# Optimization experiments

Measured on AMD Instinct MI355X. Metric: run time of the kernel, lower is better.

The kernel has to match this reference:

```python
import jax, jax.numpy as jnp
import numpy as np

B, N, D, K, L, NC = 8, 4096, 64, 8, 2, 2
EPS = 1e-5


def setup_inputs() -> dict:
    key = jax.random.key(0)
    ks = iter(jax.random.split(key, 64))
    def p(*shape, s=0.05):
        return jax.random.normal(next(ks), shape, dtype=jnp.float32) * s
    return dict(
        x=p(B, N, 3, s=1.0),
        ew1=p(3, D), eb1=jnp.zeros((D,), jnp.float32), ew2=p(D, D), eb2=jnp.zeros((D,), jnp.float32),
        wq=p(L, D, D), bq=jnp.zeros((L, D), jnp.float32), wk=p(L, D, D), bk=jnp.zeros((L, D), jnp.float32),
        wv=p(L, D, D), bv=jnp.zeros((L, D), jnp.float32),
        pw1=p(L, 3, D), pb1=jnp.zeros((L, D), jnp.float32), pw2=p(L, D, D), pb2=jnp.zeros((L, D), jnp.float32),
        aw=p(L, D), ab=jnp.zeros((L,), jnp.float32),
        ow=p(L, D, D), ob=jnp.zeros((L, D), jnp.float32),
        l1g=jnp.ones((L, D), jnp.float32), l1b=jnp.zeros((L, D), jnp.float32),
        l2g=jnp.ones((L, D), jnp.float32), l2b=jnp.zeros((L, D), jnp.float32),
        fw1=p(L, D, 2 * D), fb1=jnp.zeros((L, 2 * D), jnp.float32),
        fw2=p(L, 2 * D, D), fb2=jnp.zeros((L, D), jnp.float32),
        cw=p(D, 2 * D), cb=jnp.zeros((2 * D,), jnp.float32),
        cg=jnp.ones((2 * D,), jnp.float32), cbeta=jnp.zeros((2 * D,), jnp.float32),
        f1w=p(2 * D, 128), f1b=jnp.zeros((128,), jnp.float32),
        b1g=jnp.ones((128,), jnp.float32), b1b=jnp.zeros((128,), jnp.float32),
        f2w=p(128, 64), f2b=jnp.zeros((64,), jnp.float32),
        b2g=jnp.ones((64,), jnp.float32), b2b=jnp.zeros((64,), jnp.float32),
        f3w=p(64, NC), f3b=jnp.zeros((NC,), jnp.float32),
    )


def _ln(x, g, b):
    m = jnp.mean(x, -1, keepdims=True)
    v = jnp.mean((x - m) ** 2, -1, keepdims=True)
    return g * (x - m) * jax.lax.rsqrt(v + EPS) + b


def _bn(x, g, b):
    # eval-mode BatchNorm with running_mean=0, running_var=1
    return g * x * jax.lax.rsqrt(jnp.float32(1.0 + EPS)) + b


def _knn(pos, k):
    sq = jnp.sum(pos * pos, -1)  # [B,N]
    d2 = sq[:, :, None] - 2.0 * jnp.einsum('bnd,bmd->bnm', pos, pos) + sq[:, None, :]
    _, idx = jax.lax.top_k(-d2, k)  # k smallest distances (includes self)
    return jax.lax.stop_gradient(idx)  # [B,N,k]


def _gather(t, idx):
    b, n, k = idx.shape
    flat = idx.reshape(b, n * k)
    return jnp.take_along_axis(t, flat[:, :, None], axis=1).reshape(b, n, k, t.shape[-1])


def _block(x, pos, idx, pr):
    (wq, bq, wk, bk, wv, bv, pw1, pb1, pw2, pb2, aw, ab,
     ow, ob, l1g, l1b, l2g, l2b, fw1, fb1, fw2, fb2) = pr
    q = x @ wq + bq
    k = x @ wk + bk
    v = x @ wv + bv
    kg = _gather(k, idx)      # [B,N,K,C]
    vg = _gather(v, idx)
    pg = _gather(pos, idx)    # [B,N,K,3]
    pd = pos[:, :, None, :] - pg
    pe = jax.nn.relu(pd @ pw1 + pb1) @ pw2 + pb2
    ai = q[:, :, None, :] - kg + pe  # subtraction attention
    logits = jnp.einsum('bnkc,c->bnk', ai, aw) + ab
    w = jax.nn.softmax(logits, axis=-1)
    out = jnp.einsum('bnk,bnkc->bnc', w, vg + pe)
    out = out @ ow + ob
    out = _ln(out + x, l1g, l1b)
    ffn = jax.nn.gelu(out @ fw1 + fb1, approximate=False) @ fw2 + fb2
    return _ln(out + ffn, l2g, l2b)


def reference(x, ew1, eb1, ew2, eb2, wq, bq, wk, bk, wv, bv, pw1, pb1, pw2, pb2,
              aw, ab, ow, ob, l1g, l1b, l2g, l2b, fw1, fb1, fw2, fb2,
              cw, cb, cg, cbeta, f1w, f1b, b1g, b1b, f2w, f2b, b2g, b2b, f3w, f3b):
    pos = x
    h = jax.nn.relu(x @ ew1 + eb1) @ ew2 + eb2  # [B,N,D]
    idx = _knn(pos, K)
    stacked = (wq, bq, wk, bk, wv, bv, pw1, pb1, pw2, pb2, aw, ab,
               ow, ob, l1g, l1b, l2g, l2b, fw1, fb1, fw2, fb2)
    for i in range(L):
        h = _block(h, pos, idx, tuple(a[i] for a in stacked))
    y = jax.nn.relu(_bn(h @ cw + cb, cg, cbeta))  # [B,N,2D]
    g = jnp.max(y, axis=1)  # global max pool over points
    g = jax.nn.relu(_bn(g @ f1w + f1b, b1g, b1b))
    g = jax.nn.relu(_bn(g @ f2w + f2b, b2g, b2b))
    return g @ f3w + f3b  # [B, NC]
```

## Files before the change

kernel.cpp:

```cpp
#include <hip/hip_runtime.h>
#include <cmath>

#define BB 8
#define NN 4096
#define DD 64
#define KK 8
#define NCLS 2

constexpr float LNEPS = 1e-5f;
constexpr float BNRS = 0.9999950000374994f;
constexpr float INVSQRT2 = 0.70710678118654752440f;

constexpr int QKV_GRID = 512;
constexpr int ATTN_GRID = 1024;
constexpr int FFN_GRID = 512;

#define QPB 64
#define SPLITS 16
#define SUBSET 64

__device__ __forceinline__ float wave_sum(float v) {
#pragma unroll
  for (int m = 32; m > 0; m >>= 1) v += __shfl_xor(v, m, 64);
  return v;
}

__device__ __forceinline__ float gelu_exact(float x) {
  return 0.5f * x * (1.0f + erff(x * INVSQRT2));
}

__device__ __forceinline__ float dist2(float4 q, float4 p) {
  float dot = fmaf(q.x, p.x, fmaf(q.y, p.y, q.z * p.z));
  return fmaf(-2.0f, dot, q.w + p.w);
}

__global__ void zero_kernel(float* g) { g[threadIdx.x] = 0.0f; }

__global__ __launch_bounds__(256) void embed_kernel(
    const float* __restrict__ x, const float* __restrict__ ew1, const float* __restrict__ eb1,
    const float* __restrict__ ew2, const float* __restrict__ eb2, float* __restrict__ h) {
  __shared__ float h1[4][DD];
  int w = threadIdx.x >> 6, c = threadIdx.x & 63;
  int pt = ((blockIdx.x & 7) << 12) + (blockIdx.x >> 3) * 4 + w;
  const float* xp = x + (size_t)pt * 3;
  float x0 = xp[0], x1 = xp[1], x2 = xp[2];
  float a = fmaf(x0, ew1[c], fmaf(x1, ew1[64 + c], fmaf(x2, ew1[128 + c], eb1[c])));
  h1[w][c] = fmaxf(a, 0.0f);
  float s = eb2[c];
#pragma unroll 8
  for (int d = 0; d < DD; d++) s = fmaf(h1[w][d], ew2[d * 64 + c], s);
  h[(size_t)pt * 64 + c] = s;
}

__global__ __launch_bounds__(256) void knn_prep_kernel(const float* __restrict__ x,
                                                       float4* __restrict__ ppg) {
  int i = ((blockIdx.x & 7) << 12) + (blockIdx.x >> 3) * 256 + threadIdx.x;
  float a0 = x[3 * i + 0], a1 = x[3 * i + 1], a2 = x[3 * i + 2];
  ppg[i] = make_float4(a0, a1, a2, a0 * a0 + a1 * a1 + a2 * a2);
}

__global__ __launch_bounds__(1024) void knn_kernel(const float4* __restrict__ ppg,
                                                   int* __restrict__ idx) {
  __shared__ union {
    float v[SPLITS * 8][QPB];
    double k[SPLITS * 8][QPB];
  } mb;
  __shared__ float thrq[QPB];
  int b = blockIdx.x & 7;
  int qbase = (blockIdx.x >> 3) * QPB;
  const float4* pb = ppg + (size_t)b * NN;
  int ql = threadIdx.x & 63;
  int sp = __builtin_amdgcn_readfirstlane(threadIdx.x >> 6);
  float4 qp = pb[qbase + ql];
  const float4* cp = pb + sp * (NN / SPLITS);

  float bd[8];
#pragma unroll
  for (int u = 0; u < 8; u++) bd[u] = INFINITY;
#pragma unroll 4
  for (int jj = 0; jj < SUBSET; ++jj) {
    float d2 = dist2(qp, cp[jj]);
#pragma unroll
    for (int u = 7; u > 0; --u) bd[u] = fminf(bd[u], fmaxf(bd[u - 1], d2));
    bd[0] = fminf(bd[0], d2);
  }
#pragma unroll
  for (int u = 0; u < 8; u++) mb.v[sp * 8 + u][ql] = bd[u];
  __syncthreads();

  if (sp < 8) {
    float cd[8];
#pragma unroll
    for (int u = 0; u < 8; u++) cd[u] = INFINITY;
    int base = sp * 16;
#pragma unroll
    for (int e = 0; e < 16; e++) {
      float vv = mb.v[base + e][ql];
#pragma unroll
      for (int u = 7; u > 0; --u) cd[u] = fminf(cd[u], fmaxf(cd[u - 1], vv));
      cd[0] = fminf(cd[0], vv);
    }
#pragma unroll
    for (int u = 0; u < 8; u++) mb.v[base + u][ql] = cd[u];
  }
  __syncthreads();

  if (sp == 0) {
    float cd[8];
#pragma unroll
    for (int u = 0; u < 8; u++) cd[u] = INFINITY;
    for (int m = 0; m < 8; m++) {
      for (int e = 0; e < 8; e++) {
        float vv = mb.v[m * 16 + e][ql];
        if (__all(vv >= cd[7])) break;
#pragma unroll
        for (int u = 7; u > 0; --u) cd[u] = fminf(cd[u], fmaxf(cd[u - 1], vv));
        cd[0] = fminf(cd[0], vv);
      }
    }
    thrq[ql] = cd[7];
  }
  __syncthreads();
  float U = thrq[ql];

  double kd[8];
#pragma unroll
  for (int u = 0; u < 8; u++) kd[u] = INFINITY;
#pragma unroll 4
  for (int jj = 0; jj < NN / SPLITS; ++jj) {
    float d2 = dist2(qp, cp[jj]);
    if (d2 <= U) {
      double key = __hiloint2double(__float_as_int(d2), sp * (NN / SPLITS) + jj);
      if (key < kd[7]) {
#pragma unroll
        for (int u = 7; u > 0; --u) kd[u] = fmin(kd[u], fmax(kd[u - 1], key));
        kd[0] = fmin(kd[0], key);
      }
    }
  }
#pragma unroll
  for (int u = 0; u < 8; u++) mb.k[sp * 8 + u][ql] = kd[u];
  __syncthreads();

  if (sp < 8) {
    double cd[8];
#pragma unroll
    for (int u = 0; u < 8; u++) cd[u] = INFINITY;
    int base = sp * 16;
#pragma unroll
    for (int e = 0; e < 16; e++) {
      double key = mb.k[base + e][ql];
#pragma unroll
      for (int u = 7; u > 0; --u) cd[u] = fmin(cd[u], fmax(cd[u - 1], key));
      cd[0] = fmin(cd[0], key);
    }
#pragma unroll
    for (int u = 0; u < 8; u++) mb.k[base + u][ql] = cd[u];
  }
  __syncthreads();

  if (sp == 0) {
    double cd[8];
#pragma unroll
    for (int u = 0; u < 8; u++) cd[u] = INFINITY;
    for (int m = 0; m < 8; m++) {
      for (int e = 0; e < 8; e++) {
        double key = mb.k[m * 16 + e][ql];
        if (__all(key >= cd[7])) break;
#pragma unroll
        for (int u = 7; u > 0; --u) cd[u] = fmin(cd[u], fmax(cd[u - 1], key));
        cd[0] = fmin(cd[0], key);
      }
    }
    int* op = idx + ((size_t)b * NN + qbase + ql) * 8;
#pragma unroll
    for (int u = 0; u < 8; u++) op[u] = __double2loint(cd[u]);
  }
}

__global__ __launch_bounds__(256) void qkv_kernel(
    const float* __restrict__ h, const float* __restrict__ wq, const float* __restrict__ bq,
    const float* __restrict__ wk, const float* __restrict__ bk,
    const float* __restrict__ wv, const float* __restrict__ bv,
    float* __restrict__ q, float* __restrict__ k, float* __restrict__ v) {
  __shared__ float lwq[DD * DD], lwk[DD * DD], lwv[DD * DD];
  __shared__ float lbq[DD], lbk[DD], lbv[DD];
  __shared__ __attribute__((aligned(16))) float hb[4][DD][4];
  int tid = threadIdx.x;
  for (int i = tid; i < DD * DD; i += 256) { lwq[i] = wq[i]; lwk[i] = wk[i]; lwv[i] = wv[i]; }
  if (tid < DD) { lbq[tid] = bq[tid]; lbk[tid] = bk[tid]; lbv[tid] = bv[tid]; }
  __syncthreads();
  int w = tid >> 6, c = tid & 63;
  int batch = blockIdx.x & 7, pos = blockIdx.x >> 3;
  constexpr int ITERS = NN / ((QKV_GRID / 8) * 16);
  for (int it = 0; it < ITERS; ++it) {
    int p0 = (batch << 12) + ((it * 64 + pos) * 4 + w) * 4;
#pragma unroll
    for (int i = 0; i < 4; i++) hb[w][c][i] = h[(size_t)(p0 + i) * 64 + c];
    float aq[4], ak[4], av[4];
#pragma unroll
    for (int i = 0; i < 4; i++) { aq[i] = lbq[c]; ak[i] = lbk[c]; av[i] = lbv[c]; }
#pragma unroll 4
    for (int d = 0; d < DD; d++) {
      float wq_ = lwq[d * 64 + c], wk_ = lwk[d * 64 + c], wv_ = lwv[d * 64 + c];
      float4 hh = *(const float4*)&hb[w][d][0];
      aq[0] = fmaf(hh.x, wq_, aq[0]); aq[1] = fmaf(hh.y, wq_, aq[1]);
      aq[2] = fmaf(hh.z, wq_, aq[2]); aq[3] = fmaf(hh.w, wq_, aq[3]);
      ak[0] = fmaf(hh.x, wk_, ak[0]); ak[1] = fmaf(hh.y, wk_, ak[1]);
      ak[2] = fmaf(hh.z, wk_, ak[2]); ak[3] = fmaf(hh.w, wk_, ak[3]);
      av[0] = fmaf(hh.x, wv_, av[0]); av[1] = fmaf(hh.y, wv_, av[1]);
      av[2] = fmaf(hh.z, wv_, av[2]); av[3] = fmaf(hh.w, wv_, av[3]);
    }
#pragma unroll
    for (int i = 0; i < 4; i++) {
      q[(size_t)(p0 + i) * 64 + c] = aq[i];
      k[(size_t)(p0 + i) * 64 + c] = ak[i];
      v[(size_t)(p0 + i) * 64 + c] = av[i];
    }
  }
}

__global__ __launch_bounds__(256) void attn_kernel(
    const float* __restrict__ x, const float* __restrict__ h,
    const float* q, const float* __restrict__ kk, const float* __restrict__ vv,
    const int* __restrict__ idx,
    const float* __restrict__ pw1, const float* __restrict__ pb1,
    const float* __restrict__ pw2, const float* __restrict__ pb2,
    const float* __restrict__ aw, const float* __restrict__ ab,
    const float* __restrict__ ow, const float* __restrict__ ob,
    const float* __restrict__ l1g, const float* __restrict__ l1b,
    float* t) {
  __shared__ float lpw2[DD * DD];
  __shared__ float lpw1[3 * DD], lpb1[DD], lpb2[DD], law[DD], lob_[DD], ll1g[DD], ll1b[DD];
  __shared__ __attribute__((aligned(16))) float h1b[4][2][DD][8];
  __shared__ __attribute__((aligned(16))) float outb[4][2][DD];
  int tid = threadIdx.x;
  for (int i = tid; i < DD * DD; i += 256) lpw2[i] = pw2[i];
  if (tid < 3 * DD) lpw1[tid] = pw1[tid];
  if (tid < DD) {
    lpb1[tid] = pb1[tid]; lpb2[tid] = pb2[tid]; law[tid] = aw[tid];
    lob_[tid] = ob[tid]; ll1g[tid] = l1g[tid]; ll1b[tid] = l1b[tid];
  }
  float lab = ab[0];
  __syncthreads();
  int w = tid >> 6, c = tid & 63;
  int b = blockIdx.x & 7, pos = blockIdx.x >> 3;
  const float* xb = x + (size_t)b * NN * 3;
  constexpr int ITERS = NN / ((ATTN_GRID / 8) * 8);
  for (int it = 0; it < ITERS; ++it) {
    int n0 = ((it * 128 + pos) * 8) + w * 2;
    int p0 = (b << 12) + n0;
    float hs0 = h[(size_t)p0 * 64 + c], hs1 = h[(size_t)(p0 + 1) * 64 + c];
    float qs0 = q[(size_t)p0 * 64 + c], qs1 = q[(size_t)(p0 + 1) * 64 + c];
    int nb[2][8];
#pragma unroll
    for (int u = 0; u < 8; u++) {
      nb[0][u] = idx[(size_t)p0 * 8 + u];
      nb[1][u] = idx[(size_t)(p0 + 1) * 8 + u];
    }
    float kv0[8], kv1[8], vg0[8], vg1[8];
#pragma unroll
    for (int u = 0; u < 8; u++) {
      kv0[u] = kk[((size_t)(b << 12) + nb[0][u]) * 64 + c];
      kv1[u] = kk[((size_t)(b << 12) + nb[1][u]) * 64 + c];
      vg0[u] = vv[((size_t)(b << 12) + nb[0][u]) * 64 + c];
      vg1[u] = vv[((size_t)(b << 12) + nb[1][u]) * 64 + c];
    }
    float w1c0 = lpw1[c], w1c1 = lpw1[64 + c], w1c2 = lpw1[128 + c], b1c = lpb1[c];
#pragma unroll
    for (int pt = 0; pt < 2; ++pt) {
      int n = n0 + pt;
      float px0 = xb[n * 3 + 0], px1 = xb[n * 3 + 1], px2 = xb[n * 3 + 2];
      float h1v[8];
#pragma unroll
      for (int u = 0; u < 8; u++) {
        int m = nb[pt][u];
        float d0 = px0 - xb[m * 3 + 0], d1 = px1 - xb[m * 3 + 1], d2 = px2 - xb[m * 3 + 2];
        h1v[u] = fmaxf(fmaf(d0, w1c0, fmaf(d1, w1c1, fmaf(d2, w1c2, b1c))), 0.0f);
      }
      *(float4*)&h1b[w][pt][c][0] = make_float4(h1v[0], h1v[1], h1v[2], h1v[3]);
      *(float4*)&h1b[w][pt][c][4] = make_float4(h1v[4], h1v[5], h1v[6], h1v[7]);
    }
    float acc0[8], acc1[8];
    float pb2c = lpb2[c];
#pragma unroll
    for (int u = 0; u < 8; u++) { acc0[u] = pb2c; acc1[u] = pb2c; }
#pragma unroll 2
    for (int d = 0; d < DD; d++) {
      float wv_ = lpw2[d * 64 + c];
      float4 a0 = *(const float4*)&h1b[w][0][d][0];
      float4 b0 = *(const float4*)&h1b[w][0][d][4];
      float4 a1 = *(const float4*)&h1b[w][1][d][0];
      float4 b1 = *(const float4*)&h1b[w][1][d][4];
      acc0[0] = fmaf(a0.x, wv_, acc0[0]); acc0[1] = fmaf(a0.y, wv_, acc0[1]);
      acc0[2] = fmaf(a0.z, wv_, acc0[2]); acc0[3] = fmaf(a0.w, wv_, acc0[3]);
      acc0[4] = fmaf(b0.x, wv_, acc0[4]); acc0[5] = fmaf(b0.y, wv_, acc0[5]);
      acc0[6] = fmaf(b0.z, wv_, acc0[6]); acc0[7] = fmaf(b0.w, wv_, acc0[7]);
      acc1[0] = fmaf(a1.x, wv_, acc1[0]); acc1[1] = fmaf(a1.y, wv_, acc1[1]);
      acc1[2] = fmaf(a1.z, wv_, acc1[2]); acc1[3] = fmaf(a1.w, wv_, acc1[3]);
      acc1[4] = fmaf(b1.x, wv_, acc1[4]); acc1[5] = fmaf(b1.y, wv_, acc1[5]);
      acc1[6] = fmaf(b1.z, wv_, acc1[6]); acc1[7] = fmaf(b1.w, wv_, acc1[7]);
    }
    float lawc = law[c];
    float lg0[8], lg1[8];
#pragma unroll
    for (int u = 0; u < 8; u++) {
      lg0[u] = wave_sum((qs0 - kv0[u] + acc0[u]) * lawc) + lab;
      lg1[u] = wave_sum((qs1 - kv1[u] + acc1[u]) * lawc) + lab;
    }
    float mx0 = lg0[0], mx1 = lg1[0];
#pragma unroll
    for (int u = 1; u < 8; u++) { mx0 = fmaxf(mx0, lg0[u]); mx1 = fmaxf(mx1, lg1[u]); }
    float s0 = 0.0f, s1 = 0.0f;
#pragma unroll
    for (int u = 0; u < 8; u++) {
      lg0[u] = expf(lg0[u] - mx0); s0 += lg0[u];
      lg1[u] = expf(lg1[u] - mx1); s1 += lg1[u];
    }
    float i0 = 1.0f / s0, i1 = 1.0f / s1;
    float out0 = 0.0f, out1 = 0.0f;
#pragma unroll
    for (int u = 0; u < 8; u++) {
      out0 = fmaf(lg0[u] * i0, vg0[u] + acc0[u], out0);
      out1 = fmaf(lg1[u] * i1, vg1[u] + acc1[u], out1);
    }
    outb[w][0][c] = out0; outb[w][1][c] = out1;
    float at0 = lob_[c], at1 = at0;
#pragma unroll 4
    for (int d = 0; d < DD; d += 4) {
      float4 o0 = *(const float4*)&outb[w][0][d];
      float4 o1 = *(const float4*)&outb[w][1][d];
      float wa = ow[(d + 0) * 64 + c], wb = ow[(d + 1) * 64 + c];
      float wc = ow[(d + 2) * 64 + c], wd = ow[(d + 3) * 64 + c];
      at0 = fmaf(o0.x, wa, at0); at0 = fmaf(o0.y, wb, at0);
      at0 = fmaf(o0.z, wc, at0); at0 = fmaf(o0.w, wd, at0);
      at1 = fmaf(o1.x, wa, at1); at1 = fmaf(o1.y, wb, at1);
      at1 = fmaf(o1.z, wc, at1); at1 = fmaf(o1.w, wd, at1);
    }
    float g1c = ll1g[c], bt1c = ll1b[c];
    {
      float res = at0 + hs0;
      float mean = wave_sum(res) * (1.0f / 64.0f);
      float dv = res - mean;
      float var = wave_sum(dv * dv) * (1.0f / 64.0f);
      float ivr = 1.0f / sqrtf(var + LNEPS);
      t[(size_t)p0 * 64 + c] = fmaf(g1c, dv * ivr, bt1c);
    }
    {
      float res = at1 + hs1;
      float mean = wave_sum(res) * (1.0f / 64.0f);
      float dv = res - mean;
      float var = wave_sum(dv * dv) * (1.0f / 64.0f);
      float ivr = 1.0f / sqrtf(var + LNEPS);
      t[(size_t)(p0 + 1) * 64 + c] = fmaf(g1c, dv * ivr, bt1c);
    }
  }
}

__global__ __launch_bounds__(256) void ffn_kernel(
    const float* __restrict__ t, const float* __restrict__ fw1, const float* __restrict__ fb1,
    const float* __restrict__ fw2, const float* __restrict__ fb2,
    const float* __restrict__ l2g, const float* __restrict__ l2b, float* __restrict__ h) {
  __shared__ float lf1[DD * 128];
  __shared__ float lf2[128 * DD];
  __shared__ float lb1[128], lb2[DD], lg2[DD], lbt2[DD];
  __shared__ __attribute__((aligned(16))) float yb[4][DD][4];
  __shared__ __attribute__((aligned(16))) float hb[4][128][4];
  int tid = threadIdx.x;
  for (int i = tid; i < DD * 128; i += 256) { lf1[i] = fw1[i]; lf2[i] = fw2[i]; }
  if (tid < 128) lb1[tid] = fb1[tid];
  if (tid < DD) { lb2[tid] = fb2[tid]; lg2[tid] = l2g[tid]; lbt2[tid] = l2b[tid]; }
  __syncthreads();
  int w = tid >> 6, c = tid & 63;
  int batch = blockIdx.x & 7, pos = blockIdx.x >> 3;
  constexpr int ITERS = NN / ((FFN_GRID / 8) * 16);
  for (int it = 0; it < ITERS; ++it) {
    int p0 = (batch << 12) + ((it * 64 + pos) * 4 + w) * 4;
    float y[4];
#pragma unroll
    for (int i = 0; i < 4; i++) { y[i] = t[(size_t)(p0 + i) * 64 + c]; yb[w][c][i] = y[i]; }
    float hA[4], hB[4];
#pragma unroll
    for (int i = 0; i < 4; i++) { hA[i] = lb1[c]; hB[i] = lb1[64 + c]; }
#pragma unroll 4
    for (int d = 0; d < DD; d++) {
      float w0 = lf1[d * 128 + c], w1 = lf1[d * 128 + 64 + c];
      float4 yv = *(const float4*)&yb[w][d][0];
      hA[0] = fmaf(yv.x, w0, hA[0]); hA[1] = fmaf(yv.y, w0, hA[1]);
      hA[2] = fmaf(yv.z, w0, hA[2]); hA[3] = fmaf(yv.w, w0, hA[3]);
      hB[0] = fmaf(yv.x, w1, hB[0]); hB[1] = fmaf(yv.y, w1, hB[1]);
      hB[2] = fmaf(yv.z, w1, hB[2]); hB[3] = fmaf(yv.w, w1, hB[3]);
    }
#pragma unroll
    for (int i = 0; i < 4; i++) {
      hA[i] = gelu_exact(hA[i]); hB[i] = gelu_exact(hB[i]);
      hb[w][c][i] = hA[i]; hb[w][64 + c][i] = hB[i];
    }
    float o[4];
#pragma unroll
    for (int i = 0; i < 4; i++) o[i] = lb2[c];
#pragma unroll 4
    for (int j = 0; j < 128; j++) {
      float wv_ = lf2[j * 64 + c];
      float4 hv = *(const float4*)&hb[w][j][0];
      o[0] = fmaf(hv.x, wv_, o[0]); o[1] = fmaf(hv.y, wv_, o[1]);
      o[2] = fmaf(hv.z, wv_, o[2]); o[3] = fmaf(hv.w, wv_, o[3]);
    }
#pragma unroll
    for (int i = 0; i < 4; i++) {
      float r = y[i] + o[i];
      float mean = wave_sum(r) * (1.0f / 64.0f);
      float dv = r - mean;
      float var = wave_sum(dv * dv) * (1.0f / 64.0f);
      float ivr = 1.0f / sqrtf(var + LNEPS);
      h[(size_t)(p0 + i) * 64 + c] = fmaf(lg2[c], dv * ivr, lbt2[c]);
    }
  }
}

__global__ __launch_bounds__(256) void cls_kernel(
    const float* __restrict__ h, const float* __restrict__ cw, const float* __restrict__ cb,
    const float* __restrict__ cg, const float* __restrict__ cbeta, float* __restrict__ g) {
  __shared__ float lcw[DD * 128];
  __shared__ float lcb[128], lcg[128], lcbt[128];
  __shared__ __attribute__((aligned(16))) float hb[4][DD][4];
  __shared__ float wmax[4][128];
  int tid = threadIdx.x;
  for (int i = tid; i < DD * 128; i += 256) lcw[i] = cw[i];
  if (tid < 128) { lcb[tid] = cb[tid]; lcg[tid] = cg[tid]; lcbt[tid] = cbeta[tid]; }
  __syncthreads();
  int w = tid >> 6, c = tid & 63;
  int b = blockIdx.x & 7;
  int blk = blockIdx.x >> 3;
  int base = b * NN + blk * 32;
  float m0 = 0.0f, m1 = 0.0f;
  for (int it = 0; it < 2; ++it) {
    int p0 = base + (w * 2 + it) * 4;
#pragma unroll
    for (int i = 0; i < 4; i++) hb[w][c][i] = h[(size_t)(p0 + i) * 64 + c];
    float a0[4], a1[4];
#pragma unroll
    for (int i = 0; i < 4; i++) { a0[i] = lcb[c]; a1[i] = lcb[64 + c]; }
#pragma unroll 4
    for (int d = 0; d < DD; d++) {
      float w0 = lcw[d * 128 + c], w1 = lcw[d * 128 + 64 + c];
      float4 hv = *(const float4*)&hb[w][d][0];
      a0[0] = fmaf(hv.x, w0, a0[0]); a0[1] = fmaf(hv.y, w0, a0[1]);
      a0[2] = fmaf(hv.z, w0, a0[2]); a0[3] = fmaf(hv.w, w0, a0[3]);
      a1[0] = fmaf(hv.x, w1, a1[0]); a1[1] = fmaf(hv.y, w1, a1[1]);
      a1[2] = fmaf(hv.z, w1, a1[2]); a1[3] = fmaf(hv.w, w1, a1[3]);
    }
#pragma unroll
    for (int i = 0; i < 4; i++) {
      m0 = fmaxf(m0, fmaxf(0.0f, fmaf(lcg[c] * a0[i], BNRS, lcbt[c])));
      m1 = fmaxf(m1, fmaxf(0.0f, fmaf(lcg[64 + c] * a1[i], BNRS, lcbt[64 + c])));
    }
  }
  wmax[w][c] = m0; wmax[w][64 + c] = m1;
  __syncthreads();
  if (tid < 128) {
    float mm = fmaxf(fmaxf(wmax[0][tid], wmax[1][tid]), fmaxf(wmax[2][tid], wmax[3][tid]));
    atomicMax((int*)&g[b * 128 + tid], __float_as_int(mm));
  }
}

__global__ __launch_bounds__(128) void head_kernel(
    const float* __restrict__ g,
    const float* __restrict__ f1w, const float* __restrict__ f1b,
    const float* __restrict__ b1g, const float* __restrict__ b1b,
    const float* __restrict__ f2w, const float* __restrict__ f2b,
    const float* __restrict__ b2g, const float* __restrict__ b2b,
    const float* __restrict__ f3w, const float* __restrict__ f3b,
    float* __restrict__ out) {
  __shared__ float gb[128], g1[128], g2[64];
  int b = blockIdx.x, t = threadIdx.x;
  gb[t] = g[b * 128 + t];
  __syncthreads();
  float a = f1b[t];
#pragma unroll 4
  for (int d = 0; d < 128; d++) a = fmaf(gb[d], f1w[d * 128 + t], a);
  g1[t] = fmaxf(0.0f, fmaf(b1g[t] * a, BNRS, b1b[t]));
  __syncthreads();
  if (t < 64) {
    float a2 = f2b[t];
#pragma unroll 4
    for (int j = 0; j < 128; j++) a2 = fmaf(g1[j], f2w[j * 64 + t], a2);
    g2[t] = fmaxf(0.0f, fmaf(b2g[t] * a2, BNRS, b2b[t]));
  }
  __syncthreads();
  if (t < NCLS) {
    float a3 = f3b[t];
#pragma unroll
    for (int d = 0; d < 64; d++) a3 = fmaf(g2[d], f3w[d * NCLS + t], a3);
    out[b * NCLS + t] = a3;
  }
}

extern "C" void kernel_launch(void* const* d_in, const int* in_sizes, int n_in,
                              void* d_out, int out_size, void* d_ws, size_t ws_size,
                              hipStream_t stream) {
  const float* x    = (const float*)d_in[0];
  const float* ew1  = (const float*)d_in[1];
  const float* eb1  = (const float*)d_in[2];
  const float* ew2  = (const float*)d_in[3];
  const float* eb2  = (const float*)d_in[4];
  const float* wq   = (const float*)d_in[5];
  const float* bq   = (const float*)d_in[6];
  const float* wk   = (const float*)d_in[7];
  const float* bk   = (const float*)d_in[8];
  const float* wv   = (const float*)d_in[9];
  const float* bv   = (const float*)d_in[10];
  const float* pw1  = (const float*)d_in[11];
  const float* pb1  = (const float*)d_in[12];
  const float* pw2  = (const float*)d_in[13];
  const float* pb2  = (const float*)d_in[14];
  const float* aw   = (const float*)d_in[15];
  const float* ab   = (const float*)d_in[16];
  const float* ow   = (const float*)d_in[17];
  const float* ob   = (const float*)d_in[18];
  const float* l1g  = (const float*)d_in[19];
  const float* l1b  = (const float*)d_in[20];
  const float* l2g  = (const float*)d_in[21];
  const float* l2b  = (const float*)d_in[22];
  const float* fw1  = (const float*)d_in[23];
  const float* fb1  = (const float*)d_in[24];
  const float* fw2  = (const float*)d_in[25];
  const float* fb2  = (const float*)d_in[26];
  const float* cw   = (const float*)d_in[27];
  const float* cb   = (const float*)d_in[28];
  const float* cg   = (const float*)d_in[29];
  const float* cbeta= (const float*)d_in[30];
  const float* f1w  = (const float*)d_in[31];
  const float* f1b  = (const float*)d_in[32];
  const float* b1g  = (const float*)d_in[33];
  const float* b1b  = (const float*)d_in[34];
  const float* f2w  = (const float*)d_in[35];
  const float* f2b  = (const float*)d_in[36];
  const float* b2g  = (const float*)d_in[37];
  const float* b2b  = (const float*)d_in[38];
  const float* f3w  = (const float*)d_in[39];
  const float* f3b  = (const float*)d_in[40];

  const size_t P = (size_t)BB * NN;
  float* ws = (float*)d_ws;
  float* h = ws;
  float* q = h + P * 64;
  float* k = q + P * 64;
  float* v = k + P * 64;
  int* idx = (int*)(v + P * 64);
  float* g = (float*)(idx + P * 8);
  float4* ppg = (float4*)(g + BB * 128);
  float* t = q;

  zero_kernel<<<1, BB * 128, 0, stream>>>(g);
  embed_kernel<<<(int)(P / 4), 256, 0, stream>>>(x, ew1, eb1, ew2, eb2, h);
  knn_prep_kernel<<<(int)(P / 256), 256, 0, stream>>>(x, ppg);
  knn_kernel<<<BB * (NN / QPB), 1024, 0, stream>>>(ppg, idx);
  for (int l = 0; l < 2; l++) {
    qkv_kernel<<<QKV_GRID, 256, 0, stream>>>(h, wq + l * DD * DD, bq + l * DD,
                                             wk + l * DD * DD, bk + l * DD,
                                             wv + l * DD * DD, bv + l * DD, q, k, v);
    attn_kernel<<<ATTN_GRID, 256, 0, stream>>>(x, h, q, k, v, idx,
                                               pw1 + l * 3 * DD, pb1 + l * DD,
                                               pw2 + l * DD * DD, pb2 + l * DD,
                                               aw + l * DD, ab + l,
                                               ow + l * DD * DD, ob + l * DD,
                                               l1g + l * DD, l1b + l * DD, t);
    ffn_kernel<<<FFN_GRID, 256, 0, stream>>>(t, fw1 + l * DD * 2 * DD, fb1 + l * 2 * DD,
                                             fw2 + l * 2 * DD * DD, fb2 + l * DD,
                                             l2g + l * DD, l2b + l * DD, h);
  }
  cls_kernel<<<BB * 128, 256, 0, stream>>>(h, cw, cb, cg, cbeta, g);
  head_kernel<<<BB, 128, 0, stream>>>(g, f1w, f1b, b1g, b1b, f2w, f2b, b2g, b2b, f3w, f3b,
                                      (float*)d_out);
}
```

Measured before the change: 415.5 us.

## Run attention kernel as one wave per point pair without LDS weight staging

The attention kernel changes from 1024 persistent 256-thread blocks, which staged pw2 and the other parameters in shared memory and looped over points, to one 64-thread block per pair of points (P/2 blocks) that reads weights directly from global memory through cache. This removes the per-block weight staging and the __syncthreads barrier, and gives the scheduler many more independent waves to hide the latency of the neighbour gathers. In exchange, the 64x64 pw2 matrix is read from global/L1 for every point pair instead of from LDS, and the launch has far more blocks.

```diff
diff --git a/kernel.cpp b/kernel.cpp
--- a/kernel.cpp
+++ b/kernel.cpp
@@ -12,7 +12,6 @@
 constexpr float INVSQRT2 = 0.70710678118654752440f;
 
 constexpr int QKV_GRID = 512;
-constexpr int ATTN_GRID = 1024;
 constexpr int FFN_GRID = 512;
 
 #define QPB 64
@@ -220,7 +219,7 @@
   }
 }
 
-__global__ __launch_bounds__(256) void attn_kernel(
+__global__ __launch_bounds__(64) void attn_kernel(
     const float* __restrict__ x, const float* __restrict__ h,
     const float* q, const float* __restrict__ kk, const float* __restrict__ vv,
     const int* __restrict__ idx,
@@ -230,130 +229,115 @@
     const float* __restrict__ ow, const float* __restrict__ ob,
     const float* __restrict__ l1g, const float* __restrict__ l1b,
     float* t) {
-  __shared__ float lpw2[DD * DD];
-  __shared__ float lpw1[3 * DD], lpb1[DD], lpb2[DD], law[DD], lob_[DD], ll1g[DD], ll1b[DD];
-  __shared__ __attribute__((aligned(16))) float h1b[4][2][DD][8];
-  __shared__ __attribute__((aligned(16))) float outb[4][2][DD];
-  int tid = threadIdx.x;
-  for (int i = tid; i < DD * DD; i += 256) lpw2[i] = pw2[i];
-  if (tid < 3 * DD) lpw1[tid] = pw1[tid];
-  if (tid < DD) {
-    lpb1[tid] = pb1[tid]; lpb2[tid] = pb2[tid]; law[tid] = aw[tid];
-    lob_[tid] = ob[tid]; ll1g[tid] = l1g[tid]; ll1b[tid] = l1b[tid];
-  }
+  __shared__ __attribute__((aligned(16))) float h1b[2][DD][8];
+  __shared__ __attribute__((aligned(16))) float outb[2][DD];
+  int c = threadIdx.x;
+  int b = blockIdx.x & 7;
+  int n0 = (blockIdx.x >> 3) * 2;
+  int p0 = (b << 12) + n0;
+  const float* xb = x + (size_t)b * NN * 3;
+  float w1c0 = pw1[c], w1c1 = pw1[64 + c], w1c2 = pw1[128 + c], b1c = pb1[c];
+  float pb2c = pb2[c], lawc = aw[c], lobc = ob[c], g1c = l1g[c], bt1c = l1b[c];
   float lab = ab[0];
-  __syncthreads();
-  int w = tid >> 6, c = tid & 63;
-  int b = blockIdx.x & 7, pos = blockIdx.x >> 3;
-  const float* xb = x + (size_t)b * NN * 3;
-  constexpr int ITERS = NN / ((ATTN_GRID / 8) * 8);
-  for (int it = 0; it < ITERS; ++it) {
-    int n0 = ((it * 128 + pos) * 8) + w * 2;
-    int p0 = (b << 12) + n0;
-    float hs0 = h[(size_t)p0 * 64 + c], hs1 = h[(size_t)(p0 + 1) * 64 + c];
-    float qs0 = q[(size_t)p0 * 64 + c], qs1 = q[(size_t)(p0 + 1) * 64 + c];
-    int nb[2][8];
+  float hs0 = h[(size_t)p0 * 64 + c], hs1 = h[(size_t)(p0 + 1) * 64 + c];
+  float qs0 = q[(size_t)p0 * 64 + c], qs1 = q[(size_t)(p0 + 1) * 64 + c];
+  int nb[2][8];
+#pragma unroll
+  for (int u = 0; u < 8; u++) {
+    nb[0][u] = idx[(size_t)p0 * 8 + u];
+    nb[1][u] = idx[(size_t)(p0 + 1) * 8 + u];
+  }
+  float kv0[8], kv1[8], vg0[8], vg1[8];
+#pragma unroll
+  for (int u = 0; u < 8; u++) {
+    kv0[u] = kk[((size_t)(b << 12) + nb[0][u]) * 64 + c];
+    kv1[u] = kk[((size_t)(b << 12) + nb[1][u]) * 64 + c];
+    vg0[u] = vv[((size_t)(b << 12) + nb[0][u]) * 64 + c];
+    vg1[u] = vv[((size_t)(b << 12) + nb[1][u]) * 64 + c];
+  }
+#pragma unroll
+  for (int pt = 0; pt < 2; ++pt) {
+    int n = n0 + pt;
+    float px0 = xb[n * 3 + 0], px1 = xb[n * 3 + 1], px2 = xb[n * 3 + 2];
+    float h1v[8];
 #pragma unroll
     for (int u = 0; u < 8; u++) {
-      nb[0][u] = idx[(size_t)p0 * 8 + u];
-      nb[1][u] = idx[(size_t)(p0 + 1) * 8 + u];
-    }
-    float kv0[8], kv1[8], vg0[8], vg1[8];
-#pragma unroll
-    for (int u = 0; u < 8; u++) {
-      kv0[u] = kk[((size_t)(b << 12) + nb[0][u]) * 64 + c];
-      kv1[u] = kk[((size_t)(b << 12) + nb[1][u]) * 64 + c];
-      vg0[u] = vv[((size_t)(b << 12) + nb[0][u]) * 64 + c];
-      vg1[u] = vv[((size_t)(b << 12) + nb[1][u]) * 64 + c];
-    }
-    float w1c0 = lpw1[c], w1c1 = lpw1[64 + c], w1c2 = lpw1[128 + c], b1c = lpb1[c];
-#pragma unroll
-    for (int pt = 0; pt < 2; ++pt) {
-      int n = n0 + pt;
-      float px0 = xb[n * 3 + 0], px1 = xb[n * 3 + 1], px2 = xb[n * 3 + 2];
-      float h1v[8];
-#pragma unroll
-      for (int u = 0; u < 8; u++) {
-        int m = nb[pt][u];
-        float d0 = px0 - xb[m * 3 + 0], d1 = px1 - xb[m * 3 + 1], d2 = px2 - xb[m * 3 + 2];
-        h1v[u] = fmaxf(fmaf(d0, w1c0, fmaf(d1, w1c1, fmaf(d2, w1c2, b1c))), 0.0f);
-      }
-      *(float4*)&h1b[w][pt][c][0] = make_float4(h1v[0], h1v[1], h1v[2], h1v[3]);
-      *(float4*)&h1b[w][pt][c][4] = make_float4(h1v[4], h1v[5], h1v[6], h1v[7]);
-    }
-    float acc0[8], acc1[8];
-    float pb2c = lpb2[c];
-#pragma unroll
-    for (int u = 0; u < 8; u++) { acc0[u] = pb2c; acc1[u] = pb2c; }
+      int m = nb[pt][u];
+      float d0 = px0 - xb[m * 3 + 0], d1 = px1 - xb[m * 3 + 1], d2 = px2 - xb[m * 3 + 2];
+      h1v[u] = fmaxf(fmaf(d0, w1c0, fmaf(d1, w1c1, fmaf(d2, w1c2, b1c))), 0.0f);
+    }
+    *(float4*)&h1b[pt][c][0] = make_float4(h1v[0], h1v[1], h1v[2], h1v[3]);
+    *(float4*)&h1b[pt][c][4] = make_float4(h1v[4], h1v[5], h1v[6], h1v[7]);
+  }
+  float acc0[8], acc1[8];
+#pragma unroll
+  for (int u = 0; u < 8; u++) { acc0[u] = pb2c; acc1[u] = pb2c; }
 #pragma unroll 2
-    for (int d = 0; d < DD; d++) {
-      float wv_ = lpw2[d * 64 + c];
-      float4 a0 = *(const float4*)&h1b[w][0][d][0];
-      float4 b0 = *(const float4*)&h1b[w][0][d][4];
-      float4 a1 = *(const float4*)&h1b[w][1][d][0];
-      float4 b1 = *(const float4*)&h1b[w][1][d][4];
-      acc0[0] = fmaf(a0.x, wv_, acc0[0]); acc0[1] = fmaf(a0.y, wv_, acc0[1]);
-      acc0[2] = fmaf(a0.z, wv_, acc0[2]); acc0[3] = fmaf(a0.w, wv_, acc0[3]);
-      acc0[4] = fmaf(b0.x, wv_, acc0[4]); acc0[5] = fmaf(b0.y, wv_, acc0[5]);
-      acc0[6] = fmaf(b0.z, wv_, acc0[6]); acc0[7] = fmaf(b0.w, wv_, acc0[7]);
-      acc1[0] = fmaf(a1.x, wv_, acc1[0]); acc1[1] = fmaf(a1.y, wv_, acc1[1]);
-      acc1[2] = fmaf(a1.z, wv_, acc1[2]); acc1[3] = fmaf(a1.w, wv_, acc1[3]);
-      acc1[4] = fmaf(b1.x, wv_, acc1[4]); acc1[5] = fmaf(b1.y, wv_, acc1[5]);
-      acc1[6] = fmaf(b1.z, wv_, acc1[6]); acc1[7] = fmaf(b1.w, wv_, acc1[7]);
-    }
-    float lawc = law[c];
-    float lg0[8], lg1[8];
-#pragma unroll
-    for (int u = 0; u < 8; u++) {
-      lg0[u] = wave_sum((qs0 - kv0[u] + acc0[u]) * lawc) + lab;
-      lg1[u] = wave_sum((qs1 - kv1[u] + acc1[u]) * lawc) + lab;
-    }
-    float mx0 = lg0[0], mx1 = lg1[0];
-#pragma unroll
-    for (int u = 1; u < 8; u++) { mx0 = fmaxf(mx0, lg0[u]); mx1 = fmaxf(mx1, lg1[u]); }
-    float s0 = 0.0f, s1 = 0.0f;
-#pragma unroll
-    for (int u = 0; u < 8; u++) {
-      lg0[u] = expf(lg0[u] - mx0); s0 += lg0[u];
-      lg1[u] = expf(lg1[u] - mx1); s1 += lg1[u];
-    }
-    float i0 = 1.0f / s0, i1 = 1.0f / s1;
-    float out0 = 0.0f, out1 = 0.0f;
-#pragma unroll
-    for (int u = 0; u < 8; u++) {
-      out0 = fmaf(lg0[u] * i0, vg0[u] + acc0[u], out0);
-      out1 = fmaf(lg1[u] * i1, vg1[u] + acc1[u], out1);
-    }
-    outb[w][0][c] = out0; outb[w][1][c] = out1;
-    float at0 = lob_[c], at1 = at0;
-#pragma unroll 4
-    for (int d = 0; d < DD; d += 4) {
-      float4 o0 = *(const float4*)&outb[w][0][d];
-      float4 o1 = *(const float4*)&outb[w][1][d];
-      float wa = ow[(d + 0) * 64 + c], wb = ow[(d + 1) * 64 + c];
-      float wc = ow[(d + 2) * 64 + c], wd = ow[(d + 3) * 64 + c];
-      at0 = fmaf(o0.x, wa, at0); at0 = fmaf(o0.y, wb, at0);
-      at0 = fmaf(o0.z, wc, at0); at0 = fmaf(o0.w, wd, at0);
-      at1 = fmaf(o1.x, wa, at1); at1 = fmaf(o1.y, wb, at1);
-      at1 = fmaf(o1.z, wc, at1); at1 = fmaf(o1.w, wd, at1);
-    }
-    float g1c = ll1g[c], bt1c = ll1b[c];
-    {
-      float res = at0 + hs0;
-      float mean = wave_sum(res) * (1.0f / 64.0f);
-      float dv = res - mean;
-      float var = wave_sum(dv * dv) * (1.0f / 64.0f);
-      float ivr = 1.0f / sqrtf(var + LNEPS);
-      t[(size_t)p0 * 64 + c] = fmaf(g1c, dv * ivr, bt1c);
-    }
-    {
-      float res = at1 + hs1;
-      float mean = wave_sum(res) * (1.0f / 64.0f);
-      float dv = res - mean;
-      float var = wave_sum(dv * dv) * (1.0f / 64.0f);
-      float ivr = 1.0f / sqrtf(var + LNEPS);
-      t[(size_t)(p0 + 1) * 64 + c] = fmaf(g1c, dv * ivr, bt1c);
-    }
+  for (int d = 0; d < DD; d++) {
+    float wv_ = pw2[d * 64 + c];
+    float4 a0 = *(const float4*)&h1b[0][d][0];
+    float4 b0 = *(const float4*)&h1b[0][d][4];
+    float4 a1 = *(const float4*)&h1b[1][d][0];
+    float4 b1 = *(const float4*)&h1b[1][d][4];
+    acc0[0] = fmaf(a0.x, wv_, acc0[0]); acc0[1] = fmaf(a0.y, wv_, acc0[1]);
+    acc0[2] = fmaf(a0.z, wv_, acc0[2]); acc0[3] = fmaf(a0.w, wv_, acc0[3]);
+    acc0[4] = fmaf(b0.x, wv_, acc0[4]); acc0[5] = fmaf(b0.y, wv_, acc0[5]);
+    acc0[6] = fmaf(b0.z, wv_, acc0[6]); acc0[7] = fmaf(b0.w, wv_, acc0[7]);
+    acc1[0] = fmaf(a1.x, wv_, acc1[0]); acc1[1] = fmaf(a1.y, wv_, acc1[1]);
+    acc1[2] = fmaf(a1.z, wv_, acc1[2]); acc1[3] = fmaf(a1.w, wv_, acc1[3]);
+    acc1[4] = fmaf(b1.x, wv_, acc1[4]); acc1[5] = fmaf(b1.y, wv_, acc1[5]);
+    acc1[6] = fmaf(b1.z, wv_, acc1[6]); acc1[7] = fmaf(b1.w, wv_, acc1[7]);
+  }
+  float lg0[8], lg1[8];
+#pragma unroll
+  for (int u = 0; u < 8; u++) {
+    lg0[u] = wave_sum((qs0 - kv0[u] + acc0[u]) * lawc) + lab;
+    lg1[u] = wave_sum((qs1 - kv1[u] + acc1[u]) * lawc) + lab;
+  }
+  float mx0 = lg0[0], mx1 = lg1[0];
+#pragma unroll
+  for (int u = 1; u < 8; u++) { mx0 = fmaxf(mx0, lg0[u]); mx1 = fmaxf(mx1, lg1[u]); }
+  float s0 = 0.0f, s1 = 0.0f;
+#pragma unroll
+  for (int u = 0; u < 8; u++) {
+    lg0[u] = expf(lg0[u] - mx0); s0 += lg0[u];
+    lg1[u] = expf(lg1[u] - mx1); s1 += lg1[u];
+  }
+  float i0 = 1.0f / s0, i1 = 1.0f / s1;
+  float out0 = 0.0f, out1 = 0.0f;
+#pragma unroll
+  for (int u = 0; u < 8; u++) {
+    out0 = fmaf(lg0[u] * i0, vg0[u] + acc0[u], out0);
+    out1 = fmaf(lg1[u] * i1, vg1[u] + acc1[u], out1);
+  }
+  outb[0][c] = out0; outb[1][c] = out1;
+  float at0 = lobc, at1 = lobc;
+#pragma unroll 4
+  for (int d = 0; d < DD; d += 4) {
+    float4 o0 = *(const float4*)&outb[0][d];
+    float4 o1 = *(const float4*)&outb[1][d];
+    float wa = ow[(d + 0) * 64 + c], wb = ow[(d + 1) * 64 + c];
+    float wc = ow[(d + 2) * 64 + c], wd = ow[(d + 3) * 64 + c];
+    at0 = fmaf(o0.x, wa, at0); at0 = fmaf(o0.y, wb, at0);
+    at0 = fmaf(o0.z, wc, at0); at0 = fmaf(o0.w, wd, at0);
+    at1 = fmaf(o1.x, wa, at1); at1 = fmaf(o1.y, wb, at1);
+    at1 = fmaf(o1.z, wc, at1); at1 = fmaf(o1.w, wd, at1);
+  }
+  {
+    float res = at0 + hs0;
+    float mean = wave_sum(res) * (1.0f / 64.0f);
+    float dv = res - mean;
+    float var = wave_sum(dv * dv) * (1.0f / 64.0f);
+    float ivr = 1.0f / sqrtf(var + LNEPS);
+    t[(size_t)p0 * 64 + c] = fmaf(g1c, dv * ivr, bt1c);
+  }
+  {
+    float res = at1 + hs1;
+    float mean = wave_sum(res) * (1.0f / 64.0f);
+    float dv = res - mean;
+    float var = wave_sum(dv * dv) * (1.0f / 64.0f);
+    float ivr = 1.0f / sqrtf(var + LNEPS);
+    t[(size_t)(p0 + 1) * 64 + c] = fmaf(g1c, dv * ivr, bt1c);
   }
 }
 
@@ -560,12 +544,12 @@
     qkv_kernel<<<QKV_GRID, 256, 0, stream>>>(h, wq + l * DD * DD, bq + l * DD,
                                              wk + l * DD * DD, bk + l * DD,
                                              wv + l * DD * DD, bv + l * DD, q, k, v);
-    attn_kernel<<<ATTN_GRID, 256, 0, stream>>>(x, h, q, k, v, idx,
-                                               pw1 + l * 3 * DD, pb1 + l * DD,
-                                               pw2 + l * DD * DD, pb2 + l * DD,
-                                               aw + l * DD, ab + l,
-                                               ow + l * DD * DD, ob + l * DD,
-                                               l1g + l * DD, l1b + l * DD, t);
+    attn_kernel<<<(int)(P / 2), 64, 0, stream>>>(x, h, q, k, v, idx,
+                                                 pw1 + l * 3 * DD, pb1 + l * DD,
+                                                 pw2 + l * DD * DD, pb2 + l * DD,
+                                                 aw + l * DD, ab + l,
+                                                 ow + l * DD * DD, ob + l * DD,
+                                                 l1g + l * DD, l1b + l * DD, t);
     ffn_kernel<<<FFN_GRID, 256, 0, stream>>>(t, fw1 + l * DD * 2 * DD, fb1 + l * 2 * DD,
                                              fw2 + l * 2 * DD * DD, fb2 + l * DD,
                                              l2g + l * DD, l2b + l * DD, h);
```

Measured after the change: 387.0 us. 6.8% less time.
